# Kernel tuning notes

Hardware: AMD Instinct MI355X
Metric: run time of the kernel (lower is better)

Reference implementation:

```python
import jax, jax.numpy as jnp
import numpy as np

# ---- grid / solver constants (from opt) ----
NZ, NX = 300, 400
NPML, NPAD = 32, 0
NZP = NZ + 2 * NPML + NPAD   # 364 padded depth
NXP = NX + 2 * NPML          # 464 padded width
NSTEPS = 200
NSHOTS = 2
DX = 0.01    # km (moduli scaled by 1e-6 => velocities in km/s)
DT = 0.001   # s
SRC_Z = NPML + 2
REC_Z = NPML + 2


def _pad_model(m):
    # edge-replicate into the CPML halo + bottom pad, as ft.padding does
    return jnp.pad(m, ((NPML, NPML + NPAD), (NPML, NPML)), mode='edge')


def _sponge():
    # smooth absorbing profile in the nPml halo (sponge approximation of CPML)
    i = np.arange(NZP, dtype=np.float32)
    j = np.arange(NXP, dtype=np.float32)
    dz = np.clip(np.maximum(NPML - i, i - (NZP - 1 - NPML - NPAD)), 0, NPML) / NPML
    dx_ = np.clip(np.maximum(NPML - j, j - (NXP - 1 - NPML)), 0, NPML) / NPML
    d = dz[:, None] ** 2 + dx_[None, :] ** 2
    return jnp.asarray(np.exp(-0.1 * d), dtype=jnp.float32)


# staggered-grid finite differences (zero outside the grid)
def _dxf(f):
    return (jnp.pad(f[:, 1:], ((0, 0), (0, 1))) - f) / DX

def _dxb(f):
    return (f - jnp.pad(f[:, :-1], ((0, 0), (1, 0)))) / DX

def _dzf(f):
    return (jnp.pad(f[1:, :], ((0, 1), (0, 0))) - f) / DX

def _dzb(f):
    return (f - jnp.pad(f[:-1, :], ((1, 0), (0, 0)))) / DX


def _propagate(lam, mu, rho, stf, src_x, damp):
    """Elastic velocity-stress FDTD for one shot. stf: [NSTEPS]. Returns recs [NSTEPS, NX]."""
    lam2mu = lam + 2.0 * mu
    dt_rho = DT / rho
    zero = jnp.zeros((NZP, NXP), jnp.float32)

    def step(carry, s):
        vx, vz, sxx, szz, sxz = carry
        vx = (vx + dt_rho * (_dxf(sxx) + _dzb(sxz))) * damp
        vz = (vz + dt_rho * (_dxb(sxz) + _dzf(szz))) * damp
        dvx_dx = _dxb(vx)
        dvz_dz = _dzb(vz)
        sxx = (sxx + DT * (lam2mu * dvx_dx + lam * dvz_dz)) * damp
        szz = (szz + DT * (lam * dvx_dx + lam2mu * dvz_dz)) * damp
        sxz = (sxz + DT * mu * (_dzf(vx) + _dxf(vz))) * damp
        # explosive source injected into normal stresses
        sxx = sxx.at[SRC_Z, src_x].add(s * DT)
        szz = szz.at[SRC_Z, src_x].add(s * DT)
        rec = vx[REC_Z, NPML:NPML + NX]  # surface receiver line
        return (vx, vz, sxx, szz, sxz), rec

    init = (zero, zero, zero, zero, zero)
    _, recs = jax.lax.scan(step, init, stf)
    return recs


def _forward(Vp, Vs, Den, Stf, Mask, Shot_ids):
    Vp_pad = _pad_model(Vp)
    Vs_pad = _pad_model(Vs)
    Den_pad = _pad_model(Den)
    # masked models: gradient flows only where Mask == 1
    Vp_m = Mask * Vp_pad + (1.0 - Mask) * jax.lax.stop_gradient(Vp_pad)
    Vs_m = Mask * Vs_pad + (1.0 - Mask) * jax.lax.stop_gradient(Vs_pad)
    Den_m = Mask * Den_pad + (1.0 - Mask) * jax.lax.stop_gradient(Den_pad)
    Lam = (Vp_m ** 2 - 2.0 * Vs_m ** 2) * Den_m / 1.0e6
    Mu = Vs_m ** 2 * Den_m / 1.0e6

    damp = _sponge()
    ids = Shot_ids.astype(jnp.int32)
    src_x = NPML + 20 + ids * ((NX - 40) // NSHOTS)  # per-shot source x position
    stf = Stf[ids]                                   # [nshots, NSTEPS]
    recs = jax.vmap(lambda s, sx: _propagate(Lam, Mu, Den_m, s, sx, damp))(stf, src_x)
    return 0.5 * jnp.sum(recs.astype(jnp.float32) ** 2)  # scalar misfit


def setup_inputs() -> dict:
    key = jax.random.key(0)
    k1, k2 = jax.random.split(key)
    Vp = 2000.0 + 1500.0 * jax.random.uniform(k1, (NZ, NX), jnp.float32)   # m/s
    Vs = Vp / 1.732
    Den = 2000.0 + 500.0 * jax.random.uniform(k2, (NZ, NX), jnp.float32)   # kg/m^3
    # Ricker wavelet source, f0 = 10 Hz, shared across shots
    t = jnp.arange(NSTEPS, dtype=jnp.float32) * DT - 0.1
    f0 = 10.0
    arg = (jnp.pi * f0 * t) ** 2
    ricker = (1.0 - 2.0 * arg) * jnp.exp(-arg)
    Stf = jnp.broadcast_to(ricker, (NSHOTS, NSTEPS)).astype(jnp.float32)
    Mask = jnp.ones((NZP, NXP), jnp.float32)
    Shot_ids = jnp.arange(NSHOTS, dtype=jnp.int32)
    return {"Vp": Vp, "Vs": Vs, "Den": Den, "Stf": Stf, "Mask": Mask,
            "Shot_ids": Shot_ids, "ngpu": 1}


def reference(Vp, Vs, Den, Stf, Mask, Shot_ids, ngpu):
    return _forward(Vp, Vs, Den, Stf, Mask, Shot_ids)
```

## Files before the change

kernel.cpp:

```cpp
#include <hip/hip_runtime.h>
#include <cmath>

namespace {
constexpr int kNZ = 300, kNX = 400;
constexpr int kNPML = 32;
constexpr int kNZP = 364, kNXP = 464;
constexpr int kNSTEPS = 200, kNSHOTS = 2;
constexpr int kSRC_Z = 34, kREC_Z = 34;
constexpr float kDT = 0.001f;
constexpr float kINV_DX = 100.0f;

constexpr int kR = 4;
constexpr int kNSLAB = 92;
constexpr int kNB = kNSLAB - 1;
constexpr int kBlocks = kNSHOTS * kNSLAB;
constexpr int kThreads = 512;
constexpr int kPitch = 468;
constexpr int kFStride = kR * kPitch;

constexpr int kFlagStride = 32;
constexpr int kHaloBase = 16384;
constexpr int kHaloCount = 2 * kNSHOTS * kNB * 2 * 6 * kNXP;
constexpr int kLossOff = kHaloBase + kHaloCount;
}

__global__ void fwi_init_ws(float* __restrict__ ws) {
    const int gtid = blockIdx.x * blockDim.x + threadIdx.x;
    const int gstride = gridDim.x * blockDim.x;
    for (int q = gtid; q <= kLossOff; q += gstride) ws[q] = 0.0f;
}

__global__ __launch_bounds__(kThreads, 1) void fwi_sim_kernel(
    const float* __restrict__ Vp, const float* __restrict__ Vs,
    const float* __restrict__ Den, const float* __restrict__ Stf,
    const int* __restrict__ Shot_ids, float* __restrict__ ws) {
    __shared__ float L[4 * kFStride];
    float* Lvx  = L;
    float* Lvz  = L + kFStride;
    float* Lsxx = L + 2 * kFStride;
    float* Lsxz = L + 3 * kFStride;

    const int blk  = blockIdx.x;
    const int s    = blk / kNSLAB;
    const int slab = blk - s * kNSLAB;
    const int r0   = slab * kR;
    const int tid  = threadIdx.x;
    const bool active = tid < kNXP;
    const int lc = tid + 1;

    int*   flags = (int*)ws;
    float* halo  = ws + kHaloBase;
    float* lossp = ws + kLossOff;

    for (int q = tid; q < 4 * kFStride; q += kThreads) L[q] = 0.0f;

    auto modAt = [&](int i, int j, float& dtr_, float& dmp_, float& lam_,
                     float& mu_, float& l2m_) {
        dtr_ = dmp_ = lam_ = mu_ = l2m_ = 0.0f;
        if (i >= 0 && i < kNZP && j >= 0 && j < kNXP) {
            int iz = i - kNPML; iz = iz < 0 ? 0 : (iz > kNZ - 1 ? kNZ - 1 : iz);
            int jx = j - kNPML; jx = jx < 0 ? 0 : (jx > kNX - 1 ? kNX - 1 : jx);
            const float vp  = Vp[iz * kNX + jx];
            const float vs  = Vs[iz * kNX + jx];
            const float rho = Den[iz * kNX + jx];
            const float m = vs * vs * rho * 1e-6f;
            const float l = (vp * vp - 2.0f * vs * vs) * rho * 1e-6f;
            const float sc = kDT * kINV_DX;
            float dz = fmaxf((float)(kNPML - i), (float)(i - (kNZP - 1 - kNPML)));
            dz = fminf(fmaxf(dz, 0.0f), (float)kNPML) * (1.0f / kNPML);
            float dxx = fmaxf((float)(kNPML - j), (float)(j - (kNXP - 1 - kNPML)));
            dxx = fminf(fmaxf(dxx, 0.0f), (float)kNPML) * (1.0f / kNPML);
            dmp_ = expf(-0.1f * (dz * dz + dxx * dxx));
            dtr_ = kDT / rho * kINV_DX;
            lam_ = l * sc;
            mu_  = m * sc;
            l2m_ = (l + 2.0f * m) * sc;
        }
    };
    float rdtr[kR], rdamp[kR], rlam[kR], rmu[kR], rl2m[kR];
    float dtrT = 0, dmpT = 0, dtrB = 0, dmpB = 0;
    if (active) {
#pragma unroll
        for (int r = 0; r < kR; ++r)
            modAt(r0 + r, tid, rdtr[r], rdamp[r], rlam[r], rmu[r], rl2m[r]);
        float d0, d1, d2;
        modAt(r0 - 1, tid, dtrT, dmpT, d0, d1, d2);
        modAt(r0 + kR, tid, dtrB, dmpB, d0, d1, d2);
    }

    const int id  = Shot_ids[s];
    const int sxp = kNPML + 20 + id * ((kNX - 40) / kNSHOTS);
    const float* stf = Stf + id * kNSTEPS;
    const int rsrc = kSRC_Z - r0;
    const int rrec = kREC_Z - r0;
    const float srcm = (active && tid == sxp) ? 1.0f : 0.0f;
    const float recm = (active && (unsigned)(tid - kNPML) < (unsigned)kNX) ? 1.0f : 0.0f;

    const bool hasTop = (slab > 0);
    const bool hasBot = (slab < kNSLAB - 1);
    int* ftopw = hasTop ? &flags[((s * kNB + (slab - 1)) * 2 + 1) * kFlagStride] : nullptr;
    int* fbotw = hasBot ? &flags[((s * kNB + slab) * 2 + 0) * kFlagStride] : nullptr;
    int* ftopr = hasTop ? &flags[((s * kNB + (slab - 1)) * 2 + 0) * kFlagStride] : nullptr;
    int* fbotr = hasBot ? &flags[((s * kNB + slab) * 2 + 1) * kFlagStride] : nullptr;
    auto hbase = [&](int buf, int b, int dir) {
        return halo + ((((buf * kNSHOTS + s) * kNB + b) * 2 + dir) * 6) * kNXP;
    };

    float fvx[kR]  = {}, fvz[kR]  = {}, fsxx[kR] = {}, fszz[kR] = {}, fsxz[kR] = {};
    float rsum = 0.0f;
    __syncthreads();

    for (int t = 0; t < kNSTEPS; ++t) {
        const int rb = (t & 1) ^ 1;
        const int wb = t & 1;

        if (active) {
#pragma unroll
            for (int r = 1; r <= kR - 2; ++r) {
                const float sxxC = fsxx[r];
                const float sxzC = fsxz[r];
                const float szzC = fszz[r];
                const float sxxR = Lsxx[r * kPitch + lc + 1];
                const float sxzL = Lsxz[r * kPitch + lc - 1];
                const float nvx = (fvx[r] + rdtr[r] * ((sxxR - sxxC) + (sxzC - fsxz[r - 1]))) * rdamp[r];
                const float nvz = (fvz[r] + rdtr[r] * ((sxzC - sxzL) + (fszz[r + 1] - szzC))) * rdamp[r];
                fvx[r] = nvx;
                fvz[r] = nvz;
                Lvx[r * kPitch + lc] = nvx;
                Lvz[r * kPitch + lc] = nvz;
                if (r == rrec) rsum += recm * nvx * nvx;
            }
        }

        if (tid == 0 && hasTop) {
            while (__hip_atomic_load(ftopr, __ATOMIC_RELAXED, __HIP_MEMORY_SCOPE_AGENT) < t) {}
        }
        if (tid == 1 && hasBot) {
            while (__hip_atomic_load(fbotr, __ATOMIC_RELAXED, __HIP_MEMORY_SCOPE_AGENT) < t) {}
        }
        __syncthreads();

        float h_vxT = 0, h_vzT = 0, h_sxxT = 0, h_szzT = 0, h_sxzT = 0, h_sxz2T = 0;
        float h_sxxT_r = 0, h_sxzT_l = 0;
        float h_vxB = 0, h_vzB = 0, h_sxxB = 0, h_sxzB = 0, h_szzB = 0, h_szz2B = 0;
        float h_sxxB_r = 0, h_sxzB_l = 0;
        if (active && hasTop) {
            const float* hb = hbase(rb, slab - 1, 0);
            h_vxT   = __hip_atomic_load(hb + tid,             __ATOMIC_RELAXED, __HIP_MEMORY_SCOPE_AGENT);
            h_vzT   = __hip_atomic_load(hb + kNXP + tid,      __ATOMIC_RELAXED, __HIP_MEMORY_SCOPE_AGENT);
            h_sxxT  = __hip_atomic_load(hb + 2 * kNXP + tid,  __ATOMIC_RELAXED, __HIP_MEMORY_SCOPE_AGENT);
            h_szzT  = __hip_atomic_load(hb + 3 * kNXP + tid,  __ATOMIC_RELAXED, __HIP_MEMORY_SCOPE_AGENT);
            h_sxzT  = __hip_atomic_load(hb + 4 * kNXP + tid,  __ATOMIC_RELAXED, __HIP_MEMORY_SCOPE_AGENT);
            h_sxz2T = __hip_atomic_load(hb + 5 * kNXP + tid,  __ATOMIC_RELAXED, __HIP_MEMORY_SCOPE_AGENT);
            if (tid < kNXP - 1) h_sxxT_r = __hip_atomic_load(hb + 2 * kNXP + tid + 1, __ATOMIC_RELAXED, __HIP_MEMORY_SCOPE_AGENT);
            if (tid > 0)        h_sxzT_l = __hip_atomic_load(hb + 4 * kNXP + tid - 1, __ATOMIC_RELAXED, __HIP_MEMORY_SCOPE_AGENT);
        }
        if (active && hasBot) {
            const float* hb = hbase(rb, slab, 1);
            h_vxB   = __hip_atomic_load(hb + tid,             __ATOMIC_RELAXED, __HIP_MEMORY_SCOPE_AGENT);
            h_vzB   = __hip_atomic_load(hb + kNXP + tid,      __ATOMIC_RELAXED, __HIP_MEMORY_SCOPE_AGENT);
            h_sxxB  = __hip_atomic_load(hb + 2 * kNXP + tid,  __ATOMIC_RELAXED, __HIP_MEMORY_SCOPE_AGENT);
            h_sxzB  = __hip_atomic_load(hb + 3 * kNXP + tid,  __ATOMIC_RELAXED, __HIP_MEMORY_SCOPE_AGENT);
            h_szzB  = __hip_atomic_load(hb + 4 * kNXP + tid,  __ATOMIC_RELAXED, __HIP_MEMORY_SCOPE_AGENT);
            h_szz2B = __hip_atomic_load(hb + 5 * kNXP + tid,  __ATOMIC_RELAXED, __HIP_MEMORY_SCOPE_AGENT);
            if (tid < kNXP - 1) h_sxxB_r = __hip_atomic_load(hb + 2 * kNXP + tid + 1, __ATOMIC_RELAXED, __HIP_MEMORY_SCOPE_AGENT);
            if (tid > 0)        h_sxzB_l = __hip_atomic_load(hb + 3 * kNXP + tid - 1, __ATOMIC_RELAXED, __HIP_MEMORY_SCOPE_AGENT);
        }

        float nvxT = 0, nvzT = 0, nvxB = 0, nvzB = 0;
        if (active) {
            nvxT = (h_vxT + dtrT * ((h_sxxT_r - h_sxxT) + (h_sxzT - h_sxz2T))) * dmpT;
            nvzT = (h_vzT + dtrT * ((h_sxzT - h_sxzT_l) + (fszz[0] - h_szzT))) * dmpT;
            nvxB = (h_vxB + dtrB * ((h_sxxB_r - h_sxxB) + (h_sxzB - fsxz[kR - 1]))) * dmpB;
            nvzB = (h_vzB + dtrB * ((h_sxzB - h_sxzB_l) + (h_szz2B - h_szzB))) * dmpB;
            {
                const float sxxC = fsxx[0], sxzC = fsxz[0], szzC = fszz[0];
                const float sxxR = Lsxx[lc + 1];
                const float sxzL = Lsxz[lc - 1];
                const float nvx = (fvx[0] + rdtr[0] * ((sxxR - sxxC) + (sxzC - h_sxzT))) * rdamp[0];
                const float nvz = (fvz[0] + rdtr[0] * ((sxzC - sxzL) + (fszz[1] - szzC))) * rdamp[0];
                fvx[0] = nvx; fvz[0] = nvz;
                Lvx[lc] = nvx; Lvz[lc] = nvz;
                if (0 == rrec) rsum += recm * nvx * nvx;
            }
            {
                const int r = kR - 1;
                const float sxxC = fsxx[r], sxzC = fsxz[r], szzC = fszz[r];
                const float sxxR = Lsxx[r * kPitch + lc + 1];
                const float sxzL = Lsxz[r * kPitch + lc - 1];
                const float nvx = (fvx[r] + rdtr[r] * ((sxxR - sxxC) + (sxzC - fsxz[r - 1]))) * rdamp[r];
                const float nvz = (fvz[r] + rdtr[r] * ((sxzC - sxzL) + (h_szzB - szzC))) * rdamp[r];
                fvx[r] = nvx; fvz[r] = nvz;
                Lvx[r * kPitch + lc] = nvx; Lvz[r * kPitch + lc] = nvz;
                if (r == rrec) rsum += recm * nvx * nvx;
            }
        }
        __syncthreads();

        if (active) {
            const float sval = stf[t] * kDT;
#pragma unroll
            for (int r = 0; r < kR; ++r) {
                const float vxC = fvx[r];
                const float vzC = fvz[r];
                const float vxL = Lvx[r * kPitch + lc - 1];
                const float vzR = Lvz[r * kPitch + lc + 1];
                const float vzU = (r > 0) ? fvz[r - 1] : nvzT;
                const float vxD = (r < kR - 1) ? fvx[r + 1] : nvxB;
                const float dvx = vxC - vxL;
                const float dvz = vzC - vzU;
                float nsxx = (fsxx[r] + (rl2m[r] * dvx + rlam[r] * dvz)) * rdamp[r];
                float nszz = (fszz[r] + (rlam[r] * dvx + rl2m[r] * dvz)) * rdamp[r];
                float nsxz = (fsxz[r] + rmu[r] * ((vxD - vxC) + (vzR - vzC))) * rdamp[r];
                if (r == rsrc) { nsxx += srcm * sval; nszz += srcm * sval; }
                fsxx[r] = nsxx;
                fszz[r] = nszz;
                fsxz[r] = nsxz;
                Lsxx[r * kPitch + lc] = nsxx;
                Lsxz[r * kPitch + lc] = nsxz;
            }
            if (hasTop) {
                float* hb = hbase(wb, slab - 1, 1);
                __hip_atomic_store(hb + tid,            fvx[0],  __ATOMIC_RELAXED, __HIP_MEMORY_SCOPE_AGENT);
                __hip_atomic_store(hb + kNXP + tid,     fvz[0],  __ATOMIC_RELAXED, __HIP_MEMORY_SCOPE_AGENT);
                __hip_atomic_store(hb + 2 * kNXP + tid, fsxx[0], __ATOMIC_RELAXED, __HIP_MEMORY_SCOPE_AGENT);
                __hip_atomic_store(hb + 3 * kNXP + tid, fsxz[0], __ATOMIC_RELAXED, __HIP_MEMORY_SCOPE_AGENT);
                __hip_atomic_store(hb + 4 * kNXP + tid, fszz[0], __ATOMIC_RELAXED, __HIP_MEMORY_SCOPE_AGENT);
                __hip_atomic_store(hb + 5 * kNXP + tid, fszz[1], __ATOMIC_RELAXED, __HIP_MEMORY_SCOPE_AGENT);
            }
            if (hasBot) {
                float* hb = hbase(wb, slab, 0);
                __hip_atomic_store(hb + tid,            fvx[kR - 1],  __ATOMIC_RELAXED, __HIP_MEMORY_SCOPE_AGENT);
                __hip_atomic_store(hb + kNXP + tid,     fvz[kR - 1],  __ATOMIC_RELAXED, __HIP_MEMORY_SCOPE_AGENT);
                __hip_atomic_store(hb + 2 * kNXP + tid, fsxx[kR - 1], __ATOMIC_RELAXED, __HIP_MEMORY_SCOPE_AGENT);
                __hip_atomic_store(hb + 3 * kNXP + tid, fszz[kR - 1], __ATOMIC_RELAXED, __HIP_MEMORY_SCOPE_AGENT);
                __hip_atomic_store(hb + 4 * kNXP + tid, fsxz[kR - 1], __ATOMIC_RELAXED, __HIP_MEMORY_SCOPE_AGENT);
                __hip_atomic_store(hb + 5 * kNXP + tid, fsxz[kR - 2], __ATOMIC_RELAXED, __HIP_MEMORY_SCOPE_AGENT);
            }
        }
        __syncthreads();
        if (tid == 0 && hasTop) __hip_atomic_store(ftopw, t + 1, __ATOMIC_RELAXED, __HIP_MEMORY_SCOPE_AGENT);
        if (tid == 1 && hasBot) __hip_atomic_store(fbotw, t + 1, __ATOMIC_RELAXED, __HIP_MEMORY_SCOPE_AGENT);
    }

    for (int off = 32; off > 0; off >>= 1) rsum += __shfl_down(rsum, off, 64);
    if ((tid & 63) == 0 && rsum != 0.0f) atomicAdd(lossp, rsum);
}

__global__ void fwi_finish_kernel(const float* __restrict__ ws,
                                  float* __restrict__ out) {
    out[0] = 0.5f * ws[kLossOff];
}

extern "C" void kernel_launch(void* const* d_in, const int* in_sizes, int n_in,
                              void* d_out, int out_size, void* d_ws, size_t ws_size,
                              hipStream_t stream) {
    const float* Vp  = (const float*)d_in[0];
    const float* Vs  = (const float*)d_in[1];
    const float* Den = (const float*)d_in[2];
    const float* Stf = (const float*)d_in[3];
    const int* Shot_ids = (const int*)d_in[5];
    float* out = (float*)d_out;
    float* ws  = (float*)d_ws;

    fwi_init_ws<<<256, 256, 0, stream>>>(ws);
    void* args[] = {(void*)&Vp, (void*)&Vs, (void*)&Den, (void*)&Stf,
                    (void*)&Shot_ids, (void*)&ws};
    hipLaunchCooperativeKernel((const void*)fwi_sim_kernel, dim3(kBlocks),
                               dim3(kThreads), args, 0, stream);
    fwi_finish_kernel<<<1, 1, 0, stream>>>(ws, out);
}
```

Measured before the change: 637.8 us.

## Loosen neighbor sync by publishing full slabs and recomputing ghost rows from lagged data

Each slab now publishes its whole 4-row state into a 4-deep ring buffer and waits only until neighbors reach step t-1 instead of t. Ghost rows from one step earlier are recomputed locally, with extra model coefficients for three halo rows on each side. This gives one step of slack between neighboring blocks so stalls on the inter-block flag spin can overlap. The cost is more redundant halo arithmetic, more global atomic loads and stores per step, and two extra __syncthreads per step.

```diff
diff --git a/kernel.cpp b/kernel.cpp
--- a/kernel.cpp
+++ b/kernel.cpp
@@ -12,33 +12,37 @@
 
 constexpr int kR = 4;
 constexpr int kNSLAB = 92;
-constexpr int kNB = kNSLAB - 1;
 constexpr int kBlocks = kNSHOTS * kNSLAB;
 constexpr int kThreads = 512;
 constexpr int kPitch = 468;
-constexpr int kFStride = kR * kPitch;
+
+constexpr int kNStrips = 28;
 
 constexpr int kFlagStride = 32;
-constexpr int kHaloBase = 16384;
-constexpr int kHaloCount = 2 * kNSHOTS * kNB * 2 * 6 * kNXP;
-constexpr int kLossOff = kHaloBase + kHaloCount;
+constexpr long long kPubBase  = 8192;
+constexpr long long kPubSlab  = 5LL * kR * kNXP;
+constexpr long long kPubCount = 4LL * kNSHOTS * kNSLAB * kPubSlab;
+constexpr long long kLossOff  = kPubBase + kPubCount;
 }
 
 __global__ void fwi_init_ws(float* __restrict__ ws) {
-    const int gtid = blockIdx.x * blockDim.x + threadIdx.x;
-    const int gstride = gridDim.x * blockDim.x;
-    for (int q = gtid; q <= kLossOff; q += gstride) ws[q] = 0.0f;
+    const long long gtid = (long long)blockIdx.x * blockDim.x + threadIdx.x;
+    const long long gstride = (long long)gridDim.x * blockDim.x;
+    for (long long q = gtid; q <= kLossOff; q += gstride) ws[q] = 0.0f;
+}
+
+__device__ __forceinline__ float ald(const float* p) {
+    return __hip_atomic_load(p, __ATOMIC_RELAXED, __HIP_MEMORY_SCOPE_AGENT);
+}
+__device__ __forceinline__ void ast(float* p, float v) {
+    __hip_atomic_store(p, v, __ATOMIC_RELAXED, __HIP_MEMORY_SCOPE_AGENT);
 }
 
 __global__ __launch_bounds__(kThreads, 1) void fwi_sim_kernel(
     const float* __restrict__ Vp, const float* __restrict__ Vs,
     const float* __restrict__ Den, const float* __restrict__ Stf,
     const int* __restrict__ Shot_ids, float* __restrict__ ws) {
-    __shared__ float L[4 * kFStride];
-    float* Lvx  = L;
-    float* Lvz  = L + kFStride;
-    float* Lsxx = L + 2 * kFStride;
-    float* Lsxz = L + 3 * kFStride;
+    __shared__ float L[kNStrips * kPitch];
 
     const int blk  = blockIdx.x;
     const int s    = blk / kNSLAB;
@@ -49,10 +53,10 @@
     const int lc = tid + 1;
 
     int*   flags = (int*)ws;
-    float* halo  = ws + kHaloBase;
+    float* pub   = ws + kPubBase;
     float* lossp = ws + kLossOff;
 
-    for (int q = tid; q < 4 * kFStride; q += kThreads) L[q] = 0.0f;
+    for (int q = tid; q < kNStrips * kPitch; q += kThreads) L[q] = 0.0f;
 
     auto modAt = [&](int i, int j, float& dtr_, float& dmp_, float& lam_,
                      float& mu_, float& l2m_) {
@@ -78,14 +82,31 @@
         }
     };
     float rdtr[kR], rdamp[kR], rlam[kR], rmu[kR], rl2m[kR];
-    float dtrT = 0, dmpT = 0, dtrB = 0, dmpB = 0;
+    float gdtrT[3], gdmpT[3], gdtrB[3], gdmpB[3];
+    float tlam[2], tmu[2], tl2m[2];
+    float blam[2], bmu[2], bl2m[2];
     if (active) {
+        float d0, d1, d2, d3, d4;
 #pragma unroll
         for (int r = 0; r < kR; ++r)
             modAt(r0 + r, tid, rdtr[r], rdamp[r], rlam[r], rmu[r], rl2m[r]);
-        float d0, d1, d2;
-        modAt(r0 - 1, tid, dtrT, dmpT, d0, d1, d2);
-        modAt(r0 + kR, tid, dtrB, dmpB, d0, d1, d2);
+#pragma unroll
+        for (int i = 0; i < 3; ++i) {
+            modAt(r0 - 3 + i, tid, gdtrT[i], gdmpT[i], d0, d1, d2);
+            modAt(r0 + 4 + i, tid, gdtrB[i], gdmpB[i], d0, d1, d2);
+        }
+#pragma unroll
+        for (int j = 0; j < 2; ++j) {
+            modAt(r0 - 2 + j, tid, d3, d4, tlam[j], tmu[j], tl2m[j]);
+            modAt(r0 + 4 + j, tid, d3, d4, blam[j], bmu[j], bl2m[j]);
+        }
+    } else {
+#pragma unroll
+        for (int r = 0; r < kR; ++r) { rdtr[r]=rdamp[r]=rlam[r]=rmu[r]=rl2m[r]=0; }
+#pragma unroll
+        for (int i = 0; i < 3; ++i) { gdtrT[i]=gdmpT[i]=gdtrB[i]=gdmpB[i]=0; }
+#pragma unroll
+        for (int j = 0; j < 2; ++j) { tlam[j]=tmu[j]=tl2m[j]=blam[j]=bmu[j]=bl2m[j]=0; }
     }
 
     const int id  = Shot_ids[s];
@@ -93,106 +114,159 @@
     const float* stf = Stf + id * kNSTEPS;
     const int rsrc = kSRC_Z - r0;
     const int rrec = kREC_Z - r0;
+    const float recm = (active && (unsigned)(tid - kNPML) < (unsigned)kNX) ? 1.0f : 0.0f;
     const float srcm = (active && tid == sxp) ? 1.0f : 0.0f;
-    const float recm = (active && (unsigned)(tid - kNPML) < (unsigned)kNX) ? 1.0f : 0.0f;
 
     const bool hasTop = (slab > 0);
     const bool hasBot = (slab < kNSLAB - 1);
-    int* ftopw = hasTop ? &flags[((s * kNB + (slab - 1)) * 2 + 1) * kFlagStride] : nullptr;
-    int* fbotw = hasBot ? &flags[((s * kNB + slab) * 2 + 0) * kFlagStride] : nullptr;
-    int* ftopr = hasTop ? &flags[((s * kNB + (slab - 1)) * 2 + 0) * kFlagStride] : nullptr;
-    int* fbotr = hasBot ? &flags[((s * kNB + slab) * 2 + 1) * kFlagStride] : nullptr;
-    auto hbase = [&](int buf, int b, int dir) {
-        return halo + ((((buf * kNSHOTS + s) * kNB + b) * 2 + dir) * 6) * kNXP;
+    int* ftopr = hasTop ? &flags[(s * kNSLAB + slab - 1) * kFlagStride] : nullptr;
+    int* fbotr = hasBot ? &flags[(s * kNSLAB + slab + 1) * kFlagStride] : nullptr;
+    int* fme   = &flags[(s * kNSLAB + slab) * kFlagStride];
+    auto pbase = [&](int buf, int sl) {
+        return pub + ((long long)(buf * kNSHOTS + s) * kNSLAB + sl) * kPubSlab;
     };
-
-    float fvx[kR]  = {}, fvz[kR]  = {}, fsxx[kR] = {}, fszz[kR] = {}, fsxz[kR] = {};
+    auto Ls = [&](int strip, int c) -> float& { return L[strip * kPitch + c]; };
+
+    float fvx[kR] = {}, fvz[kR] = {}, fsxx[kR] = {}, fszz[kR] = {}, fsxz[kR] = {};
+    float szz0m1 = 0, szz0m2 = 0, sxz3m1 = 0, sxz3m2 = 0;
     float rsum = 0.0f;
     __syncthreads();
 
     for (int t = 0; t < kNSTEPS; ++t) {
-        const int rb = (t & 1) ^ 1;
-        const int wb = t & 1;
-
         if (active) {
 #pragma unroll
             for (int r = 1; r <= kR - 2; ++r) {
-                const float sxxC = fsxx[r];
-                const float sxzC = fsxz[r];
-                const float szzC = fszz[r];
-                const float sxxR = Lsxx[r * kPitch + lc + 1];
-                const float sxzL = Lsxz[r * kPitch + lc - 1];
+                const float sxxC = fsxx[r], sxzC = fsxz[r], szzC = fszz[r];
+                const float sxxR = Ls(20 + r, lc + 1);
+                const float sxzL = Ls(24 + r, lc - 1);
                 const float nvx = (fvx[r] + rdtr[r] * ((sxxR - sxxC) + (sxzC - fsxz[r - 1]))) * rdamp[r];
                 const float nvz = (fvz[r] + rdtr[r] * ((sxzC - sxzL) + (fszz[r + 1] - szzC))) * rdamp[r];
-                fvx[r] = nvx;
-                fvz[r] = nvz;
-                Lvx[r * kPitch + lc] = nvx;
-                Lvz[r * kPitch + lc] = nvz;
+                fvx[r] = nvx; fvz[r] = nvz;
+                Ls(12 + r, lc) = nvx; Ls(16 + r, lc) = nvz;
                 if (r == rrec) rsum += recm * nvx * nvx;
             }
         }
-
-        if (tid == 0 && hasTop) {
-            while (__hip_atomic_load(ftopr, __ATOMIC_RELAXED, __HIP_MEMORY_SCOPE_AGENT) < t) {}
-        }
-        if (tid == 1 && hasBot) {
-            while (__hip_atomic_load(fbotr, __ATOMIC_RELAXED, __HIP_MEMORY_SCOPE_AGENT) < t) {}
-        }
-        __syncthreads();
-
-        float h_vxT = 0, h_vzT = 0, h_sxxT = 0, h_szzT = 0, h_sxzT = 0, h_sxz2T = 0;
-        float h_sxxT_r = 0, h_sxzT_l = 0;
-        float h_vxB = 0, h_vzB = 0, h_sxxB = 0, h_sxzB = 0, h_szzB = 0, h_szz2B = 0;
-        float h_sxxB_r = 0, h_sxzB_l = 0;
+        if (t >= 2) {
+            if (tid == 0 && hasTop) {
+                while (__hip_atomic_load(ftopr, __ATOMIC_RELAXED, __HIP_MEMORY_SCOPE_AGENT) < t - 1) {}
+            }
+            if (tid == 1 && hasBot) {
+                while (__hip_atomic_load(fbotr, __ATOMIC_RELAXED, __HIP_MEMORY_SCOPE_AGENT) < t - 1) {}
+            }
+        }
+        __syncthreads();
+
+        const int rbuf = (t + 2) & 3;
+        float tvx2[3]={}, tvz2[3]={}, tsxx2[3]={}, tsxx2p[3]={}, tsxz2[4]={}, tsxz2m[3]={}, tszz2[3]={};
+        float bvx2[3]={}, bvz2[3]={}, bsxx2[3]={}, bsxx2p[3]={}, bsxz2[3]={}, bsxz2m[3]={}, bszz2[4]={};
         if (active && hasTop) {
-            const float* hb = hbase(rb, slab - 1, 0);
-            h_vxT   = __hip_atomic_load(hb + tid,             __ATOMIC_RELAXED, __HIP_MEMORY_SCOPE_AGENT);
-            h_vzT   = __hip_atomic_load(hb + kNXP + tid,      __ATOMIC_RELAXED, __HIP_MEMORY_SCOPE_AGENT);
-            h_sxxT  = __hip_atomic_load(hb + 2 * kNXP + tid,  __ATOMIC_RELAXED, __HIP_MEMORY_SCOPE_AGENT);
-            h_szzT  = __hip_atomic_load(hb + 3 * kNXP + tid,  __ATOMIC_RELAXED, __HIP_MEMORY_SCOPE_AGENT);
-            h_sxzT  = __hip_atomic_load(hb + 4 * kNXP + tid,  __ATOMIC_RELAXED, __HIP_MEMORY_SCOPE_AGENT);
-            h_sxz2T = __hip_atomic_load(hb + 5 * kNXP + tid,  __ATOMIC_RELAXED, __HIP_MEMORY_SCOPE_AGENT);
-            if (tid < kNXP - 1) h_sxxT_r = __hip_atomic_load(hb + 2 * kNXP + tid + 1, __ATOMIC_RELAXED, __HIP_MEMORY_SCOPE_AGENT);
-            if (tid > 0)        h_sxzT_l = __hip_atomic_load(hb + 4 * kNXP + tid - 1, __ATOMIC_RELAXED, __HIP_MEMORY_SCOPE_AGENT);
+            const float* b = pbase(rbuf, slab - 1);
+#pragma unroll
+            for (int i = 0; i < 3; ++i) {
+                const int m = i + 1;
+                tvx2[i]  = ald(b + (0 * 4 + m) * kNXP + tid);
+                tvz2[i]  = ald(b + (1 * 4 + m) * kNXP + tid);
+                tsxx2[i] = ald(b + (2 * 4 + m) * kNXP + tid);
+                if (tid < kNXP - 1) tsxx2p[i] = ald(b + (2 * 4 + m) * kNXP + tid + 1);
+                tszz2[i] = ald(b + (3 * 4 + m) * kNXP + tid);
+                tsxz2[m] = ald(b + (4 * 4 + m) * kNXP + tid);
+                if (tid > 0) tsxz2m[i] = ald(b + (4 * 4 + m) * kNXP + tid - 1);
+            }
+            tsxz2[0] = ald(b + (4 * 4 + 0) * kNXP + tid);
         }
         if (active && hasBot) {
-            const float* hb = hbase(rb, slab, 1);
-            h_vxB   = __hip_atomic_load(hb + tid,             __ATOMIC_RELAXED, __HIP_MEMORY_SCOPE_AGENT);
-            h_vzB   = __hip_atomic_load(hb + kNXP + tid,      __ATOMIC_RELAXED, __HIP_MEMORY_SCOPE_AGENT);
-            h_sxxB  = __hip_atomic_load(hb + 2 * kNXP + tid,  __ATOMIC_RELAXED, __HIP_MEMORY_SCOPE_AGENT);
-            h_sxzB  = __hip_atomic_load(hb + 3 * kNXP + tid,  __ATOMIC_RELAXED, __HIP_MEMORY_SCOPE_AGENT);
-            h_szzB  = __hip_atomic_load(hb + 4 * kNXP + tid,  __ATOMIC_RELAXED, __HIP_MEMORY_SCOPE_AGENT);
-            h_szz2B = __hip_atomic_load(hb + 5 * kNXP + tid,  __ATOMIC_RELAXED, __HIP_MEMORY_SCOPE_AGENT);
-            if (tid < kNXP - 1) h_sxxB_r = __hip_atomic_load(hb + 2 * kNXP + tid + 1, __ATOMIC_RELAXED, __HIP_MEMORY_SCOPE_AGENT);
-            if (tid > 0)        h_sxzB_l = __hip_atomic_load(hb + 3 * kNXP + tid - 1, __ATOMIC_RELAXED, __HIP_MEMORY_SCOPE_AGENT);
-        }
-
-        float nvxT = 0, nvzT = 0, nvxB = 0, nvzB = 0;
-        if (active) {
-            nvxT = (h_vxT + dtrT * ((h_sxxT_r - h_sxxT) + (h_sxzT - h_sxz2T))) * dmpT;
-            nvzT = (h_vzT + dtrT * ((h_sxzT - h_sxzT_l) + (fszz[0] - h_szzT))) * dmpT;
-            nvxB = (h_vxB + dtrB * ((h_sxxB_r - h_sxxB) + (h_sxzB - fsxz[kR - 1]))) * dmpB;
-            nvzB = (h_vzB + dtrB * ((h_sxzB - h_sxzB_l) + (h_szz2B - h_szzB))) * dmpB;
+            const float* b = pbase(rbuf, slab + 1);
+#pragma unroll
+            for (int i = 0; i < 3; ++i) {
+                bvx2[i]  = ald(b + (0 * 4 + i) * kNXP + tid);
+                bvz2[i]  = ald(b + (1 * 4 + i) * kNXP + tid);
+                bsxx2[i] = ald(b + (2 * 4 + i) * kNXP + tid);
+                if (tid < kNXP - 1) bsxx2p[i] = ald(b + (2 * 4 + i) * kNXP + tid + 1);
+                bszz2[i] = ald(b + (3 * 4 + i) * kNXP + tid);
+                bsxz2[i] = ald(b + (4 * 4 + i) * kNXP + tid);
+                if (tid > 0) bsxz2m[i] = ald(b + (4 * 4 + i) * kNXP + tid - 1);
+            }
+            bszz2[3] = ald(b + (3 * 4 + 3) * kNXP + tid);
+        }
+        float tvg[3] = {}, tzg[3] = {}, bvg[3] = {}, bzg[3] = {};
+        if (active) {
+#pragma unroll
+            for (int i = 0; i < 3; ++i) {
+                const int m = i + 1;
+                const float szzD = (m < 3) ? tszz2[i + 1] : szz0m2;
+                tvg[i] = (tvx2[i] + gdtrT[i] * ((tsxx2p[i] - tsxx2[i]) + (tsxz2[m] - tsxz2[m - 1]))) * gdmpT[i];
+                tzg[i] = (tvz2[i] + gdtrT[i] * ((tsxz2[m] - tsxz2m[i]) + (szzD - tszz2[i]))) * gdmpT[i];
+            }
+#pragma unroll
+            for (int i = 0; i < 3; ++i) {
+                const float sxzU = (i == 0) ? sxz3m2 : bsxz2[i - 1];
+                bvg[i] = (bvx2[i] + gdtrB[i] * ((bsxx2p[i] - bsxx2[i]) + (bsxz2[i] - sxzU))) * gdmpB[i];
+                bzg[i] = (bvz2[i] + gdtrB[i] * ((bsxz2[i] - bsxz2m[i]) + (bszz2[i + 1] - bszz2[i]))) * gdmpB[i];
+            }
+            Ls(0, lc) = tvg[1]; Ls(1, lc) = tvg[2]; Ls(2, lc) = bvg[0]; Ls(3, lc) = bvg[1];
+            Ls(4, lc) = tzg[1]; Ls(5, lc) = tzg[2]; Ls(6, lc) = bzg[0]; Ls(7, lc) = bzg[1];
+        }
+        __syncthreads();
+
+        float tsxxg[2] = {}, tszzg[2] = {}, tsxzg[2] = {};
+        float bsxxg[2] = {}, bszzg[2] = {}, bsxzg[2] = {};
+        if (active) {
+            const float sv1 = (t >= 1) ? stf[t - 1] * kDT : 0.0f;
+#pragma unroll
+            for (int j = 0; j < 2; ++j) {
+                const int m = j + 2;
+                const int i = j + 1;
+                const float dvx = tvg[i] - Ls(j, lc - 1);
+                const float dvz = tzg[i] - tzg[i - 1];
+                const float vxD = (m == 2) ? tvg[2] : fvx[0];
+                const float vzR = Ls(4 + j, lc + 1);
+                const float dmp = gdmpT[i];
+                float nsxx = (tsxx2[i] + tl2m[j] * dvx + tlam[j] * dvz) * dmp;
+                float nszz = (tszz2[i] + tlam[j] * dvx + tl2m[j] * dvz) * dmp;
+                float nsxz = (tsxz2[m] + tmu[j] * ((vxD - tvg[i]) + (vzR - tzg[i]))) * dmp;
+                if (r0 + m - 4 == kSRC_Z) { nsxx += srcm * sv1; nszz += srcm * sv1; }
+                tsxxg[j] = nsxx; tszzg[j] = nszz; tsxzg[j] = nsxz;
+            }
+#pragma unroll
+            for (int j = 0; j < 2; ++j) {
+                const int m = 8 + j;
+                const float dvx = bvg[j] - Ls(2 + j, lc - 1);
+                const float dvz = (m == 8) ? (bzg[0] - fvz[3]) : (bzg[1] - bzg[0]);
+                const float vxD = bvg[j + 1];
+                const float vzR = Ls(6 + j, lc + 1);
+                const float dmp = gdmpB[j];
+                float nsxx = (bsxx2[j] + bl2m[j] * dvx + blam[j] * dvz) * dmp;
+                float nszz = (bszz2[j] + blam[j] * dvx + bl2m[j] * dvz) * dmp;
+                float nsxz = (bsxz2[j] + bmu[j] * ((vxD - bvg[j]) + (vzR - bzg[j]))) * dmp;
+                if (r0 + m - 4 == kSRC_Z) { nsxx += srcm * sv1; nszz += srcm * sv1; }
+                bsxxg[j] = nsxx; bszzg[j] = nszz; bsxzg[j] = nsxz;
+            }
+            Ls(8, lc) = tsxxg[1]; Ls(9, lc) = bsxxg[0];
+            Ls(10, lc) = tsxzg[1]; Ls(11, lc) = bsxzg[0];
+        }
+        __syncthreads();
+
+        float gnvx3 = 0, gnvz3 = 0, gnvx8 = 0, gnvz8 = 0;
+        if (active) {
+            gnvx3 = (tvg[2] + gdtrT[2] * ((Ls(8, lc + 1) - tsxxg[1]) + (tsxzg[1] - tsxzg[0]))) * gdmpT[2];
+            gnvz3 = (tzg[2] + gdtrT[2] * ((tsxzg[1] - Ls(10, lc - 1)) + (fszz[0] - tszzg[1]))) * gdmpT[2];
+            gnvx8 = (bvg[0] + gdtrB[0] * ((Ls(9, lc + 1) - bsxxg[0]) + (bsxzg[0] - fsxz[3]))) * gdmpB[0];
+            gnvz8 = (bzg[0] + gdtrB[0] * ((bsxzg[0] - Ls(11, lc - 1)) + (bszzg[1] - bszzg[0]))) * gdmpB[0];
             {
-                const float sxxC = fsxx[0], sxzC = fsxz[0], szzC = fszz[0];
-                const float sxxR = Lsxx[lc + 1];
-                const float sxzL = Lsxz[lc - 1];
-                const float nvx = (fvx[0] + rdtr[0] * ((sxxR - sxxC) + (sxzC - h_sxzT))) * rdamp[0];
-                const float nvz = (fvz[0] + rdtr[0] * ((sxzC - sxzL) + (fszz[1] - szzC))) * rdamp[0];
+                const float sxxR = Ls(20, lc + 1), sxzL = Ls(24, lc - 1);
+                const float nvx = (fvx[0] + rdtr[0] * ((sxxR - fsxx[0]) + (fsxz[0] - tsxzg[1]))) * rdamp[0];
+                const float nvz = (fvz[0] + rdtr[0] * ((fsxz[0] - sxzL) + (fszz[1] - fszz[0]))) * rdamp[0];
                 fvx[0] = nvx; fvz[0] = nvz;
-                Lvx[lc] = nvx; Lvz[lc] = nvz;
+                Ls(12, lc) = nvx; Ls(16, lc) = nvz;
                 if (0 == rrec) rsum += recm * nvx * nvx;
             }
             {
-                const int r = kR - 1;
-                const float sxxC = fsxx[r], sxzC = fsxz[r], szzC = fszz[r];
-                const float sxxR = Lsxx[r * kPitch + lc + 1];
-                const float sxzL = Lsxz[r * kPitch + lc - 1];
-                const float nvx = (fvx[r] + rdtr[r] * ((sxxR - sxxC) + (sxzC - fsxz[r - 1]))) * rdamp[r];
-                const float nvz = (fvz[r] + rdtr[r] * ((sxzC - sxzL) + (h_szzB - szzC))) * rdamp[r];
-                fvx[r] = nvx; fvz[r] = nvz;
-                Lvx[r * kPitch + lc] = nvx; Lvz[r * kPitch + lc] = nvz;
-                if (r == rrec) rsum += recm * nvx * nvx;
+                const float sxxR = Ls(23, lc + 1), sxzL = Ls(27, lc - 1);
+                const float nvx = (fvx[3] + rdtr[3] * ((sxxR - fsxx[3]) + (fsxz[3] - fsxz[2]))) * rdamp[3];
+                const float nvz = (fvz[3] + rdtr[3] * ((fsxz[3] - sxzL) + (bszzg[0] - fszz[3]))) * rdamp[3];
+                fvx[3] = nvx; fvz[3] = nvz;
+                Ls(15, lc) = nvx; Ls(19, lc) = nvz;
+                if (3 == rrec) rsum += recm * nvx * nvx;
             }
         }
         __syncthreads();
@@ -201,46 +275,34 @@
             const float sval = stf[t] * kDT;
 #pragma unroll
             for (int r = 0; r < kR; ++r) {
-                const float vxC = fvx[r];
-                const float vzC = fvz[r];
-                const float vxL = Lvx[r * kPitch + lc - 1];
-                const float vzR = Lvz[r * kPitch + lc + 1];
-                const float vzU = (r > 0) ? fvz[r - 1] : nvzT;
-                const float vxD = (r < kR - 1) ? fvx[r + 1] : nvxB;
+                const float vxC = fvx[r], vzC = fvz[r];
+                const float vxL = Ls(12 + r, lc - 1);
+                const float vzR = Ls(16 + r, lc + 1);
+                const float vzU = (r > 0) ? fvz[r - 1] : gnvz3;
+                const float vxD = (r < kR - 1) ? fvx[r + 1] : gnvx8;
                 const float dvx = vxC - vxL;
                 const float dvz = vzC - vzU;
                 float nsxx = (fsxx[r] + (rl2m[r] * dvx + rlam[r] * dvz)) * rdamp[r];
                 float nszz = (fszz[r] + (rlam[r] * dvx + rl2m[r] * dvz)) * rdamp[r];
                 float nsxz = (fsxz[r] + rmu[r] * ((vxD - vxC) + (vzR - vzC))) * rdamp[r];
                 if (r == rsrc) { nsxx += srcm * sval; nszz += srcm * sval; }
-                fsxx[r] = nsxx;
-                fszz[r] = nszz;
-                fsxz[r] = nsxz;
-                Lsxx[r * kPitch + lc] = nsxx;
-                Lsxz[r * kPitch + lc] = nsxz;
-            }
-            if (hasTop) {
-                float* hb = hbase(wb, slab - 1, 1);
-                __hip_atomic_store(hb + tid,            fvx[0],  __ATOMIC_RELAXED, __HIP_MEMORY_SCOPE_AGENT);
-                __hip_atomic_store(hb + kNXP + tid,     fvz[0],  __ATOMIC_RELAXED, __HIP_MEMORY_SCOPE_AGENT);
-                __hip_atomic_store(hb + 2 * kNXP + tid, fsxx[0], __ATOMIC_RELAXED, __HIP_MEMORY_SCOPE_AGENT);
-                __hip_atomic_store(hb + 3 * kNXP + tid, fsxz[0], __ATOMIC_RELAXED, __HIP_MEMORY_SCOPE_AGENT);
-                __hip_atomic_store(hb + 4 * kNXP + tid, fszz[0], __ATOMIC_RELAXED, __HIP_MEMORY_SCOPE_AGENT);
-                __hip_atomic_store(hb + 5 * kNXP + tid, fszz[1], __ATOMIC_RELAXED, __HIP_MEMORY_SCOPE_AGENT);
-            }
-            if (hasBot) {
-                float* hb = hbase(wb, slab, 0);
-                __hip_atomic_store(hb + tid,            fvx[kR - 1],  __ATOMIC_RELAXED, __HIP_MEMORY_SCOPE_AGENT);
-                __hip_atomic_store(hb + kNXP + tid,     fvz[kR - 1],  __ATOMIC_RELAXED, __HIP_MEMORY_SCOPE_AGENT);
-                __hip_atomic_store(hb + 2 * kNXP + tid, fsxx[kR - 1], __ATOMIC_RELAXED, __HIP_MEMORY_SCOPE_AGENT);
-                __hip_atomic_store(hb + 3 * kNXP + tid, fszz[kR - 1], __ATOMIC_RELAXED, __HIP_MEMORY_SCOPE_AGENT);
-                __hip_atomic_store(hb + 4 * kNXP + tid, fsxz[kR - 1], __ATOMIC_RELAXED, __HIP_MEMORY_SCOPE_AGENT);
-                __hip_atomic_store(hb + 5 * kNXP + tid, fsxz[kR - 2], __ATOMIC_RELAXED, __HIP_MEMORY_SCOPE_AGENT);
-            }
-        }
-        __syncthreads();
-        if (tid == 0 && hasTop) __hip_atomic_store(ftopw, t + 1, __ATOMIC_RELAXED, __HIP_MEMORY_SCOPE_AGENT);
-        if (tid == 1 && hasBot) __hip_atomic_store(fbotw, t + 1, __ATOMIC_RELAXED, __HIP_MEMORY_SCOPE_AGENT);
+                fsxx[r] = nsxx; fszz[r] = nszz; fsxz[r] = nsxz;
+                Ls(20 + r, lc) = nsxx; Ls(24 + r, lc) = nsxz;
+            }
+            float* b = pbase(t & 3, slab);
+#pragma unroll
+            for (int r = 0; r < kR; ++r) {
+                ast(b + (0 * 4 + r) * kNXP + tid, fvx[r]);
+                ast(b + (1 * 4 + r) * kNXP + tid, fvz[r]);
+                ast(b + (2 * 4 + r) * kNXP + tid, fsxx[r]);
+                ast(b + (3 * 4 + r) * kNXP + tid, fszz[r]);
+                ast(b + (4 * 4 + r) * kNXP + tid, fsxz[r]);
+            }
+            szz0m2 = szz0m1; szz0m1 = fszz[0];
+            sxz3m2 = sxz3m1; sxz3m1 = fsxz[3];
+        }
+        __syncthreads();
+        if (tid == 0) __hip_atomic_store(fme, t + 1, __ATOMIC_RELAXED, __HIP_MEMORY_SCOPE_AGENT);
     }
 
     for (int off = 32; off > 0; off >>= 1) rsum += __shfl_down(rsum, off, 64);
@@ -263,7 +325,7 @@
     float* out = (float*)d_out;
     float* ws  = (float*)d_ws;
 
-    fwi_init_ws<<<256, 256, 0, stream>>>(ws);
+    fwi_init_ws<<<512, 256, 0, stream>>>(ws);
     void* args[] = {(void*)&Vp, (void*)&Vs, (void*)&Den, (void*)&Stf,
                     (void*)&Shot_ids, (void*)&ws};
     hipLaunchCooperativeKernel((const void*)fwi_sim_kernel, dim3(kBlocks),
```

Result: slower. 869.1 us (+36.3%).
